# Optimization experiments

Measured on AMD Instinct MI355X. Metric: run time of the kernel, lower is better.

Reference implementation:

```python
import jax, jax.numpy as jnp
import numpy as np

B, S, D, E, K = 4, 2048, 1024, 8, 2
EPS, W_THRES, TEMP = 1e-4, 0.1, 1.0


def setup_inputs() -> dict:
    key = jax.random.key(0)
    k1, k2, k3, k4, k5 = jax.random.split(key, 5)
    x = jax.random.normal(k1, (B, S, D), dtype=jnp.float32)
    gate_W = jax.random.normal(k2, (D, E), dtype=jnp.float32) * 0.02
    gate_b = jnp.zeros((E,), dtype=jnp.float32)
    expert_W = jax.random.normal(k3, (E, D, D), dtype=jnp.float32) * 0.02
    expert_b = jnp.zeros((E, D), dtype=jnp.float32)
    return {"x": x, "gate_W": gate_W, "gate_b": gate_b,
            "expert_W": expert_W, "expert_b": expert_b}


def reference(x, gate_W, gate_b, expert_W, expert_b):
    # Gating: linear -> temperature -> clamp-min(eps) -> softmax
    scores = jnp.maximum((x @ gate_W + gate_b) / TEMP, EPS)      # [B,S,E]
    p = jax.nn.softmax(scores, axis=-1)                           # [B,S,E]
    _, topk_idx = jax.lax.top_k(p, K)                             # [B,S,K]
    # boolean membership mask of selected experts
    topk_mask = jax.nn.one_hot(topk_idx, E, dtype=p.dtype).sum(-2) > 0  # [B,S,E]
    # weights: clamp-min(weight_thres), normalized by detached sum over selected
    w = jnp.maximum(p, W_THRES)                                   # [B,S,E]
    w_gather = jnp.take_along_axis(w, topk_idx, axis=-1)          # [B,S,K]
    total = jax.lax.stop_gradient(w_gather.sum(-1, keepdims=True))
    w = w / total
    comb = jnp.where(topk_mask, w, jnp.zeros_like(w))             # [B,S,E]
    # Dense equivalent of gather/expert/scatter loop (E small): each expert
    # is Linear(D, D); masked combine weights zero out unselected experts.
    y = jnp.einsum('bsd,edf->bsef', x, expert_W) + expert_b       # [B,S,E,D]
    out = jnp.einsum('bsef,bse->bsf', y, comb) / K                # [B,S,D]
    return out
```

## Files before the change

kernel.cpp:

```cpp
#include <hip/hip_runtime.h>
#include <hip/hip_fp16.h>
#include <stdint.h>

#define TOK 8192
#define DIM 1024
#define NE 8
#define NT 72
#define NCT 8

typedef short bf16x8 __attribute__((ext_vector_type(8)));
typedef float f32x4 __attribute__((ext_vector_type(4)));

__device__ __forceinline__ unsigned short f2bf(float f) {
  unsigned int u = __float_as_uint(f);
  u += 0x7FFFu + ((u >> 16) & 1u);
  return (unsigned short)(u >> 16);
}

__device__ __forceinline__ void gl_lds16(const void* g, void* l) {
  __builtin_amdgcn_global_load_lds(
      (__attribute__((address_space(1))) unsigned int*)(g),
      (__attribute__((address_space(3))) unsigned int*)(l), 16, 0, 0);
}

__device__ __forceinline__ unsigned lds_off(const void* p) {
  return (unsigned)(size_t)(__attribute__((address_space(3))) const void*)p;
}

__global__ __launch_bounds__(256) void gate_kernel(
    const float* __restrict__ x, const float* __restrict__ gW,
    const float* __restrict__ gb, unsigned short* __restrict__ xb,
    int* __restrict__ eSel, float* __restrict__ wSel, int* __restrict__ cnt)
{
  if (blockIdx.x == 0 && threadIdx.x < NE) cnt[threadIdx.x] = 0;

  __shared__ float gWs[NE * DIM];
#pragma unroll
  for (int h = 0; h < 8; ++h) {
    const int m = threadIdx.x + h * 256;
    float4 v = ((const float4*)gW)[m];
    const int d = m >> 1, e0 = (m & 1) * 4;
    gWs[(e0 + 0) * DIM + d] = v.x;
    gWs[(e0 + 1) * DIM + d] = v.y;
    gWs[(e0 + 2) * DIM + d] = v.z;
    gWs[(e0 + 3) * DIM + d] = v.w;
  }
  __syncthreads();

  const int wave = threadIdx.x >> 6;
  const int lane = threadIdx.x & 63;
  const int t = blockIdx.x * 4 + wave;
  const float4* xrow = (const float4*)(x + (size_t)t * DIM);
  ushort4* xbrow = (ushort4*)(xb + (size_t)t * DIM);

  double acc[NE];
#pragma unroll
  for (int e = 0; e < NE; ++e) acc[e] = 0.0;

#pragma unroll
  for (int i = 0; i < 4; ++i) {
    const int j = i * 64 + lane;
    float4 v = xrow[j];
    ushort4 pk;
    pk.x = f2bf(v.x); pk.y = f2bf(v.y); pk.z = f2bf(v.z); pk.w = f2bf(v.w);
    xbrow[j] = pk;
#pragma unroll
    for (int e = 0; e < NE; ++e) {
      float4 gv = *(const float4*)&gWs[e * DIM + j * 4];
      acc[e] += (double)v.x * (double)gv.x + (double)v.y * (double)gv.y
              + (double)v.z * (double)gv.z + (double)v.w * (double)gv.w;
    }
  }
#pragma unroll
  for (int off = 32; off > 0; off >>= 1) {
#pragma unroll
    for (int e = 0; e < NE; ++e)
      acc[e] += __shfl_xor(acc[e], off, 64);
  }

  if (lane == 0) {
    double s[NE];
#pragma unroll
    for (int e = 0; e < NE; ++e) {
      s[e] = acc[e] + (double)gb[e];
      if (s[e] < 1e-4) s[e] = 1e-4;
    }
    int e0 = 0;
    for (int e = 1; e < NE; ++e) if (s[e] > s[e0]) e0 = e;
    int e1 = (e0 == 0) ? 1 : 0;
    for (int e = 0; e < NE; ++e) if (e != e0 && s[e] > s[e1]) e1 = e;
    float m = (float)s[e0];
    float Z = 0.f, pf[NE];
#pragma unroll
    for (int e = 0; e < NE; ++e) { pf[e] = __expf((float)s[e] - m); Z += pf[e]; }
    float w0 = pf[e0] / Z; if (w0 < 0.1f) w0 = 0.1f;
    float w1 = pf[e1] / Z; if (w1 < 0.1f) w1 = 0.1f;
    const float inv = 0.5f / (w0 + w1);
    eSel[t * 2 + 0] = e0;
    eSel[t * 2 + 1] = e1;
    wSel[t * 2 + 0] = w0 * inv;
    wSel[t * 2 + 1] = w1 * inv;
  }
}

__global__ __launch_bounds__(256) void scatter_kernel(
    const int* __restrict__ eSel, const float* __restrict__ wSel,
    int* __restrict__ cnt, int* __restrict__ listTok, float* __restrict__ listW)
{
  __shared__ int lcnt[NE];
  __shared__ int base[NE];
  const int tid = threadIdx.x;
  if (tid < NE) lcnt[tid] = 0;
  __syncthreads();

  const int t = blockIdx.x * 256 + tid;
  const int e0 = eSel[t * 2 + 0];
  const int e1 = eSel[t * 2 + 1];
  const float w0 = wSel[t * 2 + 0];
  const float w1 = wSel[t * 2 + 1];
  const int l0 = atomicAdd(&lcnt[e0], 1);
  const int l1 = atomicAdd(&lcnt[e1], 1);
  __syncthreads();
  if (tid < NE) base[tid] = atomicAdd(&cnt[tid], lcnt[tid]);
  __syncthreads();

  const int p0 = base[e0] + l0;
  listTok[e0 * TOK + p0] = t * 2 + 0;
  listW [e0 * TOK + p0] = w0;
  const int p1 = base[e1] + l1;
  listTok[e1 * TOK + p1] = t * 2 + 1;
  listW [e1 * TOK + p1] = w1;
}

__global__ __launch_bounds__(256) void transpose_w(
    const float* __restrict__ W, unsigned short* __restrict__ Wt)
{
  __shared__ float t2[64][65];
  const int b  = blockIdx.x;
  const int e  = b >> 8;
  const int db = (b >> 4) & 15;
  const int fb = b & 15;
  const int d0 = db * 64, f0 = fb * 64;
  const int tid = threadIdx.x;
#pragma unroll
  for (int h = 0; h < 4; ++h) {
    const int idx = tid + h * 256;
    const int r = idx >> 4, c4 = idx & 15;
    float4 v = *(const float4*)&W[((size_t)e * DIM + d0 + r) * DIM + f0 + c4 * 4];
    t2[r][c4 * 4 + 0] = v.x;
    t2[r][c4 * 4 + 1] = v.y;
    t2[r][c4 * 4 + 2] = v.z;
    t2[r][c4 * 4 + 3] = v.w;
  }
  __syncthreads();
#pragma unroll
  for (int h = 0; h < 8; ++h) {
    const int o = tid + h * 256;
    const int f = o >> 5, k2 = (o & 31) * 2;
    const unsigned int lo = f2bf(t2[k2][f]);
    const unsigned int hi = f2bf(t2[k2 + 1][f]);
    *(unsigned int*)&Wt[((size_t)e * DIM + f0 + f) * DIM + d0 + k2] =
        lo | (hi << 16);
  }
}

#define WAITVM(n) asm volatile("s_waitcnt vmcnt(" #n ")" ::: "memory")

#define STG(kt, bs)                                                          \
  { const int off_ = (kt) * 32;                                              \
    gl_lds16(srcA0 + off_, &As[bs][w * 2048 + 0]);                           \
    gl_lds16(srcA1 + off_, &As[bs][w * 2048 + 512]);                         \
    gl_lds16(srcA2 + off_, &As[bs][w * 2048 + 1024]);                        \
    gl_lds16(srcA3 + off_, &As[bs][w * 2048 + 1536]);                        \
    gl_lds16(srcB0 + off_, &Bs[bs][w * 1024 + 0]);                           \
    gl_lds16(srcB1 + off_, &Bs[bs][w * 1024 + 512]); }

#define CMP(bs)                                                              \
  { const unsigned aA = asOff + (unsigned)(bs) * 16384u + rdA2;              \
    const unsigned bA = bsOff + (unsigned)(bs) * 8192u + rdB2;               \
    bf16x8 a0,a1,a2,a3,a4,a5,a6,a7,b0,b1,b2,b3;                              \
    asm volatile(                                                            \
      "ds_read_b128 %0, %12 offset:0\n\t"                                    \
      "ds_read_b128 %1, %12 offset:1024\n\t"                                 \
      "ds_read_b128 %2, %12 offset:2048\n\t"                                 \
      "ds_read_b128 %3, %12 offset:3072\n\t"                                 \
      "ds_read_b128 %4, %12 offset:4096\n\t"                                 \
      "ds_read_b128 %5, %12 offset:5120\n\t"                                 \
      "ds_read_b128 %6, %12 offset:6144\n\t"                                 \
      "ds_read_b128 %7, %12 offset:7168\n\t"                                 \
      "ds_read_b128 %8, %13 offset:0\n\t"                                    \
      "ds_read_b128 %9, %13 offset:1024\n\t"                                 \
      "ds_read_b128 %10, %13 offset:2048\n\t"                                \
      "ds_read_b128 %11, %13 offset:3072\n\t"                                \
      "s_waitcnt lgkmcnt(0)"                                                 \
      : "=&v"(a0),"=&v"(a1),"=&v"(a2),"=&v"(a3),                             \
        "=&v"(a4),"=&v"(a5),"=&v"(a6),"=&v"(a7),                             \
        "=&v"(b0),"=&v"(b1),"=&v"(b2),"=&v"(b3)                              \
      : "v"(aA), "v"(bA)                                                     \
      : "memory");                                                           \
    __builtin_amdgcn_sched_barrier(0);                                       \
    bf16x8 af[8] = {a0, a1, a2, a3, a4, a5, a6, a7};                         \
    bf16x8 bfr[4] = {b0, b1, b2, b3};                                        \
    __builtin_amdgcn_s_setprio(1);                                           \
    _Pragma("unroll")                                                        \
    for (int mt = 0; mt < 8; ++mt)                                           \
      _Pragma("unroll")                                                      \
      for (int nt = 0; nt < 4; ++nt)                                         \
        acc[mt][nt] = __builtin_amdgcn_mfma_f32_16x16x32_bf16(               \
            af[mt], bfr[nt], acc[mt][nt], 0, 0, 0);                          \
    __builtin_amdgcn_s_setprio(0); }

__global__ __launch_bounds__(256, 2) void moe_gemm(
    const unsigned short* __restrict__ xb, const unsigned short* __restrict__ Wt,
    const float* __restrict__ eb, const int* __restrict__ cnt,
    const int* __restrict__ listTok, const float* __restrict__ listW,
    __half* __restrict__ yslot)
{
  const int dId = blockIdx.x % NT;
  const int cT  = blockIdx.x / NT;
  int e = -1, r0 = 0, rows = 0, accT = 0;
#pragma unroll
  for (int ee = 0; ee < NE; ++ee) {
    const int c = cnt[ee];
    const int nt = (c + 255) >> 8;
    if (dId >= accT && dId < accT + nt) {
      e = ee; r0 = (dId - accT) * 256;
      rows = c - r0; if (rows > 256) rows = 256;
    }
    accT += nt;
  }
  if (e < 0) return;

  __shared__ __align__(16) unsigned short As[3][256 * 32];
  __shared__ __align__(16) unsigned short Bs[3][128 * 32];
  __shared__ int   tid_s[256];
  __shared__ float w_s[256];

  const int tid = threadIdx.x;
  if (tid < rows) {
    tid_s[tid] = listTok[e * TOK + r0 + tid];
    w_s[tid]   = listW [e * TOK + r0 + tid];
  } else {
    tid_s[tid] = 0;
    w_s[tid]   = 0.0f;
  }
  __syncthreads();

  const int w    = tid >> 6;
  const int lane = tid & 63;
  const int qsrc = (lane & 3) ^ ((lane >> 3) & 3);
  const int lr   = lane >> 2;
  const unsigned short* srcA0 = xb + (size_t)(tid_s[w * 64 +  0 + lr] >> 1) * DIM + qsrc * 8;
  const unsigned short* srcA1 = xb + (size_t)(tid_s[w * 64 + 16 + lr] >> 1) * DIM + qsrc * 8;
  const unsigned short* srcA2 = xb + (size_t)(tid_s[w * 64 + 32 + lr] >> 1) * DIM + qsrc * 8;
  const unsigned short* srcA3 = xb + (size_t)(tid_s[w * 64 + 48 + lr] >> 1) * DIM + qsrc * 8;
  const unsigned short* srcB0 = Wt + ((size_t)e * DIM + cT * 128 + w * 32 +  0 + lr) * DIM + qsrc * 8;
  const unsigned short* srcB1 = Wt + ((size_t)e * DIM + cT * 128 + w * 32 + 16 + lr) * DIM + qsrc * 8;

  const int wr = w >> 1, wc = w & 1;
  const int mrow = lane & 15;
  const int qg   = lane >> 4;
  const int s8   = (qg ^ ((mrow >> 1) & 3)) * 8;
  const unsigned rdA2 = (unsigned)(((wr * 128 + mrow) * 32 + s8) * 2);
  const unsigned rdB2 = (unsigned)(((wc * 64 + mrow) * 32 + s8) * 2);
  const unsigned asOff = lds_off(&As[0][0]);
  const unsigned bsOff = lds_off(&Bs[0][0]);

  f32x4 acc[8][4];
#pragma unroll
  for (int i = 0; i < 8; ++i)
#pragma unroll
    for (int j = 0; j < 4; ++j)
      acc[i][j] = {0.f, 0.f, 0.f, 0.f};

  STG(0, 0);
  STG(1, 1);
  WAITVM(6);
  __builtin_amdgcn_s_barrier();

  int bC = 0, bS = 2;
#pragma unroll 1
  for (int kt = 0; kt < 30; ++kt) {
    STG(kt + 2, bS);
    CMP(bC);
    WAITVM(6);
    __builtin_amdgcn_s_barrier();
    bC = (bC == 2) ? 0 : bC + 1;
    bS = (bS == 2) ? 0 : bS + 1;
  }
  CMP(0);
  WAITVM(0);
  __builtin_amdgcn_s_barrier();
  CMP(1);

  const int colBase = cT * 128 + wc * 64 + mrow;
  float bias[4];
#pragma unroll
  for (int nt = 0; nt < 4; ++nt)
    bias[nt] = eb[(size_t)e * DIM + colBase + nt * 16];
#pragma unroll
  for (int mt = 0; mt < 8; ++mt) {
#pragma unroll
    for (int r = 0; r < 4; ++r) {
      const int rloc = wr * 128 + mt * 16 + (lane >> 4) * 4 + r;
      if (rloc < rows) {
        const int tk    = tid_s[rloc];
        const float wgt = w_s[rloc];
        __half* dst = yslot + ((size_t)(tk & 1) * TOK + (size_t)(tk >> 1)) * DIM;
#pragma unroll
        for (int nt = 0; nt < 4; ++nt)
          dst[colBase + nt * 16] = __float2half(wgt * (acc[mt][nt][r] + bias[nt]));
      }
    }
  }
}

__global__ __launch_bounds__(256) void combine(
    const __half* __restrict__ y0, const __half* __restrict__ y1,
    float4* __restrict__ out)
{
  const size_t i = (size_t)blockIdx.x * 256 + threadIdx.x;
  const ushort4 ua = ((const ushort4*)y0)[i];
  const ushort4 ub = ((const ushort4*)y1)[i];
  const __half* ah = (const __half*)&ua;
  const __half* bh = (const __half*)&ub;
  float4 o;
  o.x = __half2float(ah[0]) + __half2float(bh[0]);
  o.y = __half2float(ah[1]) + __half2float(bh[1]);
  o.z = __half2float(ah[2]) + __half2float(bh[2]);
  o.w = __half2float(ah[3]) + __half2float(bh[3]);
  out[i] = o;
}

extern "C" void kernel_launch(void* const* d_in, const int* in_sizes, int n_in,
                              void* d_out, int out_size, void* d_ws, size_t ws_size,
                              hipStream_t stream)
{
  const float* x  = (const float*)d_in[0];
  const float* gW = (const float*)d_in[1];
  const float* gb = (const float*)d_in[2];
  const float* eW = (const float*)d_in[3];
  const float* eb = (const float*)d_in[4];
  float* out = (float*)d_out;

  char* p = (char*)d_ws;
  unsigned short* xb = (unsigned short*)p;  p += (size_t)TOK * DIM * 2;
  unsigned short* Wt = (unsigned short*)p;  p += (size_t)NE * DIM * DIM * 2;
  __half* yslot = (__half*)p;               p += (size_t)2 * TOK * DIM * 2;
  int* cnt = (int*)p;                       p += 256;
  int* listTok = (int*)p;                   p += (size_t)NE * TOK * 4;
  float* listW = (float*)p;                 p += (size_t)NE * TOK * 4;

  int*   eSel = (int*)yslot;
  float* wSel = (float*)((char*)yslot + TOK * 8);

  gate_kernel<<<TOK / 4, 256, 0, stream>>>(x, gW, gb, xb, eSel, wSel, cnt);
  scatter_kernel<<<TOK / 256, 256, 0, stream>>>(eSel, wSel, cnt, listTok, listW);
  transpose_w<<<NE * 256, 256, 0, stream>>>(eW, Wt);
  moe_gemm<<<NT * NCT, 256, 0, stream>>>(xb, Wt, eb, cnt, listTok, listW, yslot);
  combine<<<TOK * DIM / 4 / 256, 256, 0, stream>>>(
      yslot, yslot + (size_t)TOK * DIM, (float4*)out);
}
```

Before: 198.8 us.

## Widen MoE GEMM tile to 256x256, double-buffer, and fuse transpose into gate

Each MoE GEMM block now computes 256 output columns instead of 128, halving column tiles and doubling per-wave accumulators to 8x8 MFMA tiles for more reuse of the A (token) data loaded from LDS. The LDS pipeline changes from triple buffering with two stages in flight to double buffering with a full vmcnt(0) wait each step. The LDS reads are split so half the MFMAs can start before all fragments arrive. The weight transpose kernel is merged into the gate kernel as extra blocks, saving one launch and letting both overlap. The larger accumulator raises register pressure at two blocks per CU, and the shallower prefetch may expose more memory latency.

```diff
diff --git a/kernel.cpp b/kernel.cpp
--- a/kernel.cpp
+++ b/kernel.cpp
@@ -6,7 +6,7 @@
 #define DIM 1024
 #define NE 8
 #define NT 72
-#define NCT 8
+#define NCT 4
 
 typedef short bf16x8 __attribute__((ext_vector_type(8)));
 typedef float f32x4 __attribute__((ext_vector_type(4)));
@@ -27,14 +27,48 @@
   return (unsigned)(size_t)(__attribute__((address_space(3))) const void*)p;
 }
 
-__global__ __launch_bounds__(256) void gate_kernel(
+__global__ __launch_bounds__(256) void gate_transpose(
     const float* __restrict__ x, const float* __restrict__ gW,
     const float* __restrict__ gb, unsigned short* __restrict__ xb,
-    int* __restrict__ eSel, float* __restrict__ wSel, int* __restrict__ cnt)
-{
+    int* __restrict__ eSel, float* __restrict__ wSel, int* __restrict__ cnt,
+    const float* __restrict__ W, unsigned short* __restrict__ Wt)
+{
+  __shared__ __align__(16) float smem[NE * DIM];
+
+  if (blockIdx.x >= 2048) {
+    float (*t2)[65] = (float(*)[65])smem;
+    const int b  = blockIdx.x - 2048;
+    const int e  = b >> 8;
+    const int db = (b >> 4) & 15;
+    const int fb = b & 15;
+    const int d0 = db * 64, f0 = fb * 64;
+    const int tid = threadIdx.x;
+#pragma unroll
+    for (int h = 0; h < 4; ++h) {
+      const int idx = tid + h * 256;
+      const int r = idx >> 4, c4 = idx & 15;
+      float4 v = *(const float4*)&W[((size_t)e * DIM + d0 + r) * DIM + f0 + c4 * 4];
+      t2[r][c4 * 4 + 0] = v.x;
+      t2[r][c4 * 4 + 1] = v.y;
+      t2[r][c4 * 4 + 2] = v.z;
+      t2[r][c4 * 4 + 3] = v.w;
+    }
+    __syncthreads();
+#pragma unroll
+    for (int h = 0; h < 8; ++h) {
+      const int o = tid + h * 256;
+      const int f = o >> 5, k2 = (o & 31) * 2;
+      const unsigned int lo = f2bf(t2[k2][f]);
+      const unsigned int hi = f2bf(t2[k2 + 1][f]);
+      *(unsigned int*)&Wt[((size_t)e * DIM + f0 + f) * DIM + d0 + k2] =
+          lo | (hi << 16);
+    }
+    return;
+  }
+
   if (blockIdx.x == 0 && threadIdx.x < NE) cnt[threadIdx.x] = 0;
 
-  __shared__ float gWs[NE * DIM];
+  float* gWs = smem;
 #pragma unroll
   for (int h = 0; h < 8; ++h) {
     const int m = threadIdx.x + h * 256;
@@ -132,38 +166,6 @@
   listW [e1 * TOK + p1] = w1;
 }
 
-__global__ __launch_bounds__(256) void transpose_w(
-    const float* __restrict__ W, unsigned short* __restrict__ Wt)
-{
-  __shared__ float t2[64][65];
-  const int b  = blockIdx.x;
-  const int e  = b >> 8;
-  const int db = (b >> 4) & 15;
-  const int fb = b & 15;
-  const int d0 = db * 64, f0 = fb * 64;
-  const int tid = threadIdx.x;
-#pragma unroll
-  for (int h = 0; h < 4; ++h) {
-    const int idx = tid + h * 256;
-    const int r = idx >> 4, c4 = idx & 15;
-    float4 v = *(const float4*)&W[((size_t)e * DIM + d0 + r) * DIM + f0 + c4 * 4];
-    t2[r][c4 * 4 + 0] = v.x;
-    t2[r][c4 * 4 + 1] = v.y;
-    t2[r][c4 * 4 + 2] = v.z;
-    t2[r][c4 * 4 + 3] = v.w;
-  }
-  __syncthreads();
-#pragma unroll
-  for (int h = 0; h < 8; ++h) {
-    const int o = tid + h * 256;
-    const int f = o >> 5, k2 = (o & 31) * 2;
-    const unsigned int lo = f2bf(t2[k2][f]);
-    const unsigned int hi = f2bf(t2[k2 + 1][f]);
-    *(unsigned int*)&Wt[((size_t)e * DIM + f0 + f) * DIM + d0 + k2] =
-        lo | (hi << 16);
-  }
-}
-
 #define WAITVM(n) asm volatile("s_waitcnt vmcnt(" #n ")" ::: "memory")
 
 #define STG(kt, bs)                                                          \
@@ -172,42 +174,60 @@
     gl_lds16(srcA1 + off_, &As[bs][w * 2048 + 512]);                         \
     gl_lds16(srcA2 + off_, &As[bs][w * 2048 + 1024]);                        \
     gl_lds16(srcA3 + off_, &As[bs][w * 2048 + 1536]);                        \
-    gl_lds16(srcB0 + off_, &Bs[bs][w * 1024 + 0]);                           \
-    gl_lds16(srcB1 + off_, &Bs[bs][w * 1024 + 512]); }
+    gl_lds16(srcB0 + off_, &Bs[bs][w * 2048 + 0]);                           \
+    gl_lds16(srcB1 + off_, &Bs[bs][w * 2048 + 512]);                         \
+    gl_lds16(srcB2 + off_, &Bs[bs][w * 2048 + 1024]);                        \
+    gl_lds16(srcB3 + off_, &Bs[bs][w * 2048 + 1536]); }
 
 #define CMP(bs)                                                              \
   { const unsigned aA = asOff + (unsigned)(bs) * 16384u + rdA2;              \
-    const unsigned bA = bsOff + (unsigned)(bs) * 8192u + rdB2;               \
-    bf16x8 a0,a1,a2,a3,a4,a5,a6,a7,b0,b1,b2,b3;                              \
+    const unsigned bA = bsOff + (unsigned)(bs) * 16384u + rdB2;              \
+    bf16x8 a0,a1,a2,a3,a4,a5,a6,a7,b0,b1,b2,b3,b4,b5,b6,b7;                  \
     asm volatile(                                                            \
-      "ds_read_b128 %0, %12 offset:0\n\t"                                    \
-      "ds_read_b128 %1, %12 offset:1024\n\t"                                 \
-      "ds_read_b128 %2, %12 offset:2048\n\t"                                 \
-      "ds_read_b128 %3, %12 offset:3072\n\t"                                 \
-      "ds_read_b128 %4, %12 offset:4096\n\t"                                 \
-      "ds_read_b128 %5, %12 offset:5120\n\t"                                 \
-      "ds_read_b128 %6, %12 offset:6144\n\t"                                 \
-      "ds_read_b128 %7, %12 offset:7168\n\t"                                 \
-      "ds_read_b128 %8, %13 offset:0\n\t"                                    \
-      "ds_read_b128 %9, %13 offset:1024\n\t"                                 \
-      "ds_read_b128 %10, %13 offset:2048\n\t"                                \
-      "ds_read_b128 %11, %13 offset:3072\n\t"                                \
-      "s_waitcnt lgkmcnt(0)"                                                 \
+      "ds_read_b128 %0, %16 offset:0\n\t"                                    \
+      "ds_read_b128 %1, %16 offset:1024\n\t"                                 \
+      "ds_read_b128 %2, %16 offset:2048\n\t"                                 \
+      "ds_read_b128 %3, %16 offset:3072\n\t"                                 \
+      "ds_read_b128 %8, %17 offset:0\n\t"                                    \
+      "ds_read_b128 %9, %17 offset:1024\n\t"                                 \
+      "ds_read_b128 %10, %17 offset:2048\n\t"                                \
+      "ds_read_b128 %11, %17 offset:3072\n\t"                                \
+      "ds_read_b128 %12, %17 offset:4096\n\t"                                \
+      "ds_read_b128 %13, %17 offset:5120\n\t"                                \
+      "ds_read_b128 %14, %17 offset:6144\n\t"                                \
+      "ds_read_b128 %15, %17 offset:7168\n\t"                                \
+      "ds_read_b128 %4, %16 offset:4096\n\t"                                 \
+      "ds_read_b128 %5, %16 offset:5120\n\t"                                 \
+      "ds_read_b128 %6, %16 offset:6144\n\t"                                 \
+      "ds_read_b128 %7, %16 offset:7168\n\t"                                 \
+      "s_waitcnt lgkmcnt(4)"                                                 \
       : "=&v"(a0),"=&v"(a1),"=&v"(a2),"=&v"(a3),                             \
         "=&v"(a4),"=&v"(a5),"=&v"(a6),"=&v"(a7),                             \
-        "=&v"(b0),"=&v"(b1),"=&v"(b2),"=&v"(b3)                              \
+        "=&v"(b0),"=&v"(b1),"=&v"(b2),"=&v"(b3),                             \
+        "=&v"(b4),"=&v"(b5),"=&v"(b6),"=&v"(b7)                              \
       : "v"(aA), "v"(bA)                                                     \
       : "memory");                                                           \
     __builtin_amdgcn_sched_barrier(0);                                       \
-    bf16x8 af[8] = {a0, a1, a2, a3, a4, a5, a6, a7};                         \
-    bf16x8 bfr[4] = {b0, b1, b2, b3};                                        \
+    bf16x8 afL[4] = {a0, a1, a2, a3};                                        \
+    bf16x8 afH[4] = {a4, a5, a6, a7};                                        \
+    bf16x8 bfr[8] = {b0, b1, b2, b3, b4, b5, b6, b7};                        \
     __builtin_amdgcn_s_setprio(1);                                           \
     _Pragma("unroll")                                                        \
-    for (int mt = 0; mt < 8; ++mt)                                           \
+    for (int mt = 0; mt < 4; ++mt)                                           \
       _Pragma("unroll")                                                      \
-      for (int nt = 0; nt < 4; ++nt)                                         \
+      for (int nt = 0; nt < 8; ++nt)                                         \
         acc[mt][nt] = __builtin_amdgcn_mfma_f32_16x16x32_bf16(               \
-            af[mt], bfr[nt], acc[mt][nt], 0, 0, 0);                          \
+            afL[mt], bfr[nt], acc[mt][nt], 0, 0, 0);                         \
+    __builtin_amdgcn_s_setprio(0);                                           \
+    asm volatile("s_waitcnt lgkmcnt(0)" ::: "memory");                       \
+    __builtin_amdgcn_sched_barrier(0);                                       \
+    __builtin_amdgcn_s_setprio(1);                                           \
+    _Pragma("unroll")                                                        \
+    for (int mt = 0; mt < 4; ++mt)                                           \
+      _Pragma("unroll")                                                      \
+      for (int nt = 0; nt < 8; ++nt)                                         \
+        acc[mt + 4][nt] = __builtin_amdgcn_mfma_f32_16x16x32_bf16(           \
+            afH[mt], bfr[nt], acc[mt + 4][nt], 0, 0, 0);                     \
     __builtin_amdgcn_s_setprio(0); }
 
 __global__ __launch_bounds__(256, 2) void moe_gemm(
@@ -231,8 +251,8 @@
   }
   if (e < 0) return;
 
-  __shared__ __align__(16) unsigned short As[3][256 * 32];
-  __shared__ __align__(16) unsigned short Bs[3][128 * 32];
+  __shared__ __align__(16) unsigned short As[2][256 * 32];
+  __shared__ __align__(16) unsigned short Bs[2][256 * 32];
   __shared__ int   tid_s[256];
   __shared__ float w_s[256];
 
@@ -254,49 +274,48 @@
   const unsigned short* srcA1 = xb + (size_t)(tid_s[w * 64 + 16 + lr] >> 1) * DIM + qsrc * 8;
   const unsigned short* srcA2 = xb + (size_t)(tid_s[w * 64 + 32 + lr] >> 1) * DIM + qsrc * 8;
   const unsigned short* srcA3 = xb + (size_t)(tid_s[w * 64 + 48 + lr] >> 1) * DIM + qsrc * 8;
-  const unsigned short* srcB0 = Wt + ((size_t)e * DIM + cT * 128 + w * 32 +  0 + lr) * DIM + qsrc * 8;
-  const unsigned short* srcB1 = Wt + ((size_t)e * DIM + cT * 128 + w * 32 + 16 + lr) * DIM + qsrc * 8;
+  const size_t bbase = ((size_t)e * DIM + cT * 256 + w * 64) * DIM;
+  const unsigned short* srcB0 = Wt + bbase + (size_t)( 0 + lr) * DIM + qsrc * 8;
+  const unsigned short* srcB1 = Wt + bbase + (size_t)(16 + lr) * DIM + qsrc * 8;
+  const unsigned short* srcB2 = Wt + bbase + (size_t)(32 + lr) * DIM + qsrc * 8;
+  const unsigned short* srcB3 = Wt + bbase + (size_t)(48 + lr) * DIM + qsrc * 8;
 
   const int wr = w >> 1, wc = w & 1;
   const int mrow = lane & 15;
   const int qg   = lane >> 4;
   const int s8   = (qg ^ ((mrow >> 1) & 3)) * 8;
   const unsigned rdA2 = (unsigned)(((wr * 128 + mrow) * 32 + s8) * 2);
-  const unsigned rdB2 = (unsigned)(((wc * 64 + mrow) * 32 + s8) * 2);
+  const unsigned rdB2 = (unsigned)(((wc * 128 + mrow) * 32 + s8) * 2);
   const unsigned asOff = lds_off(&As[0][0]);
   const unsigned bsOff = lds_off(&Bs[0][0]);
 
-  f32x4 acc[8][4];
+  f32x4 acc[8][8];
 #pragma unroll
   for (int i = 0; i < 8; ++i)
 #pragma unroll
-    for (int j = 0; j < 4; ++j)
+    for (int j = 0; j < 8; ++j)
       acc[i][j] = {0.f, 0.f, 0.f, 0.f};
 
   STG(0, 0);
-  STG(1, 1);
-  WAITVM(6);
-  __builtin_amdgcn_s_barrier();
-
-  int bC = 0, bS = 2;
-#pragma unroll 1
-  for (int kt = 0; kt < 30; ++kt) {
-    STG(kt + 2, bS);
-    CMP(bC);
-    WAITVM(6);
-    __builtin_amdgcn_s_barrier();
-    bC = (bC == 2) ? 0 : bC + 1;
-    bS = (bS == 2) ? 0 : bS + 1;
-  }
-  CMP(0);
   WAITVM(0);
   __builtin_amdgcn_s_barrier();
-  CMP(1);
-
-  const int colBase = cT * 128 + wc * 64 + mrow;
-  float bias[4];
-#pragma unroll
-  for (int nt = 0; nt < 4; ++nt)
+
+  int buf = 0;
+#pragma unroll 1
+  for (int kt = 0; kt < 32; ++kt) {
+    if (kt < 31) STG(kt + 1, buf ^ 1);
+    CMP(buf);
+    if (kt < 31) {
+      WAITVM(0);
+      __builtin_amdgcn_s_barrier();
+      buf ^= 1;
+    }
+  }
+
+  const int colBase = cT * 256 + wc * 128 + mrow;
+  float bias[8];
+#pragma unroll
+  for (int nt = 0; nt < 8; ++nt)
     bias[nt] = eb[(size_t)e * DIM + colBase + nt * 16];
 #pragma unroll
   for (int mt = 0; mt < 8; ++mt) {
@@ -308,7 +327,7 @@
         const float wgt = w_s[rloc];
         __half* dst = yslot + ((size_t)(tk & 1) * TOK + (size_t)(tk >> 1)) * DIM;
 #pragma unroll
-        for (int nt = 0; nt < 4; ++nt)
+        for (int nt = 0; nt < 8; ++nt)
           dst[colBase + nt * 16] = __float2half(wgt * (acc[mt][nt][r] + bias[nt]));
       }
     }
@@ -354,9 +373,8 @@
   int*   eSel = (int*)yslot;
   float* wSel = (float*)((char*)yslot + TOK * 8);
 
-  gate_kernel<<<TOK / 4, 256, 0, stream>>>(x, gW, gb, xb, eSel, wSel, cnt);
+  gate_transpose<<<4096, 256, 0, stream>>>(x, gW, gb, xb, eSel, wSel, cnt, eW, Wt);
   scatter_kernel<<<TOK / 256, 256, 0, stream>>>(eSel, wSel, cnt, listTok, listW);
-  transpose_w<<<NE * 256, 256, 0, stream>>>(eW, Wt);
   moe_gemm<<<NT * NCT, 256, 0, stream>>>(xb, Wt, eb, cnt, listTok, listW, yslot);
   combine<<<TOK * DIM / 4 / 256, 256, 0, stream>>>(
       yslot, yslot + (size_t)TOK * DIM, (float4*)out);
```

Result: slower. 483.3 us (+143.0%).

## Enlarge MoE GEMM tile to 256x256 with 8 waves and fuse weight transpose into gate

Applied to the files above, without the earlier changes.

The grouped GEMM now uses 512-thread blocks computing 256x256 output tiles (NCT halved to 4), so each staged A tile is reused across twice as many output columns and fewer blocks are launched. The LDS reads are split so the first half of the MFMAs can start after a partial lgkmcnt wait. The weight transpose kernel is merged into the gate kernel as extra blocks to remove one launch and let the two overlap. The larger tile doubles the B LDS buffers, and the 512-thread blocks with launch_bounds(512,2) may cut occupancy or raise register pressure.

```diff
diff --git a/kernel.cpp b/kernel.cpp
--- a/kernel.cpp
+++ b/kernel.cpp
@@ -6,7 +6,7 @@
 #define DIM 1024
 #define NE 8
 #define NT 72
-#define NCT 8
+#define NCT 4
 
 typedef short bf16x8 __attribute__((ext_vector_type(8)));
 typedef float f32x4 __attribute__((ext_vector_type(4)));
@@ -27,14 +27,48 @@
   return (unsigned)(size_t)(__attribute__((address_space(3))) const void*)p;
 }
 
-__global__ __launch_bounds__(256) void gate_kernel(
+__global__ __launch_bounds__(256) void gate_transpose(
     const float* __restrict__ x, const float* __restrict__ gW,
     const float* __restrict__ gb, unsigned short* __restrict__ xb,
-    int* __restrict__ eSel, float* __restrict__ wSel, int* __restrict__ cnt)
-{
+    int* __restrict__ eSel, float* __restrict__ wSel, int* __restrict__ cnt,
+    const float* __restrict__ W, unsigned short* __restrict__ Wt)
+{
+  __shared__ __align__(16) float smem[NE * DIM];
+
+  if (blockIdx.x >= 2048) {
+    float (*t2)[65] = (float(*)[65])smem;
+    const int b  = blockIdx.x - 2048;
+    const int e  = b >> 8;
+    const int db = (b >> 4) & 15;
+    const int fb = b & 15;
+    const int d0 = db * 64, f0 = fb * 64;
+    const int tid = threadIdx.x;
+#pragma unroll
+    for (int h = 0; h < 4; ++h) {
+      const int idx = tid + h * 256;
+      const int r = idx >> 4, c4 = idx & 15;
+      float4 v = *(const float4*)&W[((size_t)e * DIM + d0 + r) * DIM + f0 + c4 * 4];
+      t2[r][c4 * 4 + 0] = v.x;
+      t2[r][c4 * 4 + 1] = v.y;
+      t2[r][c4 * 4 + 2] = v.z;
+      t2[r][c4 * 4 + 3] = v.w;
+    }
+    __syncthreads();
+#pragma unroll
+    for (int h = 0; h < 8; ++h) {
+      const int o = tid + h * 256;
+      const int f = o >> 5, k2 = (o & 31) * 2;
+      const unsigned int lo = f2bf(t2[k2][f]);
+      const unsigned int hi = f2bf(t2[k2 + 1][f]);
+      *(unsigned int*)&Wt[((size_t)e * DIM + f0 + f) * DIM + d0 + k2] =
+          lo | (hi << 16);
+    }
+    return;
+  }
+
   if (blockIdx.x == 0 && threadIdx.x < NE) cnt[threadIdx.x] = 0;
 
-  __shared__ float gWs[NE * DIM];
+  float* gWs = smem;
 #pragma unroll
   for (int h = 0; h < 8; ++h) {
     const int m = threadIdx.x + h * 256;
@@ -132,85 +166,62 @@
   listW [e1 * TOK + p1] = w1;
 }
 
-__global__ __launch_bounds__(256) void transpose_w(
-    const float* __restrict__ W, unsigned short* __restrict__ Wt)
-{
-  __shared__ float t2[64][65];
-  const int b  = blockIdx.x;
-  const int e  = b >> 8;
-  const int db = (b >> 4) & 15;
-  const int fb = b & 15;
-  const int d0 = db * 64, f0 = fb * 64;
-  const int tid = threadIdx.x;
-#pragma unroll
-  for (int h = 0; h < 4; ++h) {
-    const int idx = tid + h * 256;
-    const int r = idx >> 4, c4 = idx & 15;
-    float4 v = *(const float4*)&W[((size_t)e * DIM + d0 + r) * DIM + f0 + c4 * 4];
-    t2[r][c4 * 4 + 0] = v.x;
-    t2[r][c4 * 4 + 1] = v.y;
-    t2[r][c4 * 4 + 2] = v.z;
-    t2[r][c4 * 4 + 3] = v.w;
-  }
-  __syncthreads();
-#pragma unroll
-  for (int h = 0; h < 8; ++h) {
-    const int o = tid + h * 256;
-    const int f = o >> 5, k2 = (o & 31) * 2;
-    const unsigned int lo = f2bf(t2[k2][f]);
-    const unsigned int hi = f2bf(t2[k2 + 1][f]);
-    *(unsigned int*)&Wt[((size_t)e * DIM + f0 + f) * DIM + d0 + k2] =
-        lo | (hi << 16);
-  }
-}
-
 #define WAITVM(n) asm volatile("s_waitcnt vmcnt(" #n ")" ::: "memory")
 
 #define STG(kt, bs)                                                          \
   { const int off_ = (kt) * 32;                                              \
-    gl_lds16(srcA0 + off_, &As[bs][w * 2048 + 0]);                           \
-    gl_lds16(srcA1 + off_, &As[bs][w * 2048 + 512]);                         \
-    gl_lds16(srcA2 + off_, &As[bs][w * 2048 + 1024]);                        \
-    gl_lds16(srcA3 + off_, &As[bs][w * 2048 + 1536]);                        \
-    gl_lds16(srcB0 + off_, &Bs[bs][w * 1024 + 0]);                           \
-    gl_lds16(srcB1 + off_, &Bs[bs][w * 1024 + 512]); }
+    gl_lds16(srcA0 + off_, &As[bs][w * 512]);                                \
+    gl_lds16(srcA1 + off_, &As[bs][128 * 32 + w * 512]);                     \
+    gl_lds16(srcB0 + off_, &Bs[bs][w * 512]);                                \
+    gl_lds16(srcB1 + off_, &Bs[bs][128 * 32 + w * 512]); }
 
 #define CMP(bs)                                                              \
   { const unsigned aA = asOff + (unsigned)(bs) * 16384u + rdA2;              \
-    const unsigned bA = bsOff + (unsigned)(bs) * 8192u + rdB2;               \
+    const unsigned bA = bsOff + (unsigned)(bs) * 16384u + rdB2;              \
     bf16x8 a0,a1,a2,a3,a4,a5,a6,a7,b0,b1,b2,b3;                              \
     asm volatile(                                                            \
       "ds_read_b128 %0, %12 offset:0\n\t"                                    \
       "ds_read_b128 %1, %12 offset:1024\n\t"                                 \
       "ds_read_b128 %2, %12 offset:2048\n\t"                                 \
       "ds_read_b128 %3, %12 offset:3072\n\t"                                 \
+      "ds_read_b128 %8, %13 offset:0\n\t"                                    \
+      "ds_read_b128 %9, %13 offset:1024\n\t"                                 \
+      "ds_read_b128 %10, %13 offset:2048\n\t"                                \
+      "ds_read_b128 %11, %13 offset:3072\n\t"                                \
       "ds_read_b128 %4, %12 offset:4096\n\t"                                 \
       "ds_read_b128 %5, %12 offset:5120\n\t"                                 \
       "ds_read_b128 %6, %12 offset:6144\n\t"                                 \
       "ds_read_b128 %7, %12 offset:7168\n\t"                                 \
-      "ds_read_b128 %8, %13 offset:0\n\t"                                    \
-      "ds_read_b128 %9, %13 offset:1024\n\t"                                 \
-      "ds_read_b128 %10, %13 offset:2048\n\t"                                \
-      "ds_read_b128 %11, %13 offset:3072\n\t"                                \
-      "s_waitcnt lgkmcnt(0)"                                                 \
+      "s_waitcnt lgkmcnt(4)"                                                 \
       : "=&v"(a0),"=&v"(a1),"=&v"(a2),"=&v"(a3),                             \
         "=&v"(a4),"=&v"(a5),"=&v"(a6),"=&v"(a7),                             \
         "=&v"(b0),"=&v"(b1),"=&v"(b2),"=&v"(b3)                              \
       : "v"(aA), "v"(bA)                                                     \
       : "memory");                                                           \
     __builtin_amdgcn_sched_barrier(0);                                       \
-    bf16x8 af[8] = {a0, a1, a2, a3, a4, a5, a6, a7};                         \
+    bf16x8 afL[4] = {a0, a1, a2, a3};                                        \
+    bf16x8 afH[4] = {a4, a5, a6, a7};                                        \
     bf16x8 bfr[4] = {b0, b1, b2, b3};                                        \
     __builtin_amdgcn_s_setprio(1);                                           \
     _Pragma("unroll")                                                        \
-    for (int mt = 0; mt < 8; ++mt)                                           \
+    for (int mt = 0; mt < 4; ++mt)                                           \
       _Pragma("unroll")                                                      \
       for (int nt = 0; nt < 4; ++nt)                                         \
         acc[mt][nt] = __builtin_amdgcn_mfma_f32_16x16x32_bf16(               \
-            af[mt], bfr[nt], acc[mt][nt], 0, 0, 0);                          \
+            afL[mt], bfr[nt], acc[mt][nt], 0, 0, 0);                         \
+    __builtin_amdgcn_s_setprio(0);                                           \
+    asm volatile("s_waitcnt lgkmcnt(0)" ::: "memory");                       \
+    __builtin_amdgcn_sched_barrier(0);                                       \
+    __builtin_amdgcn_s_setprio(1);                                           \
+    _Pragma("unroll")                                                        \
+    for (int mt = 0; mt < 4; ++mt)                                           \
+      _Pragma("unroll")                                                      \
+      for (int nt = 0; nt < 4; ++nt)                                         \
+        acc[mt + 4][nt] = __builtin_amdgcn_mfma_f32_16x16x32_bf16(           \
+            afH[mt], bfr[nt], acc[mt + 4][nt], 0, 0, 0);                     \
     __builtin_amdgcn_s_setprio(0); }
 
-__global__ __launch_bounds__(256, 2) void moe_gemm(
+__global__ __launch_bounds__(512, 2) void moe_gemm(
     const unsigned short* __restrict__ xb, const unsigned short* __restrict__ Wt,
     const float* __restrict__ eb, const int* __restrict__ cnt,
     const int* __restrict__ listTok, const float* __restrict__ listW,
@@ -232,17 +243,19 @@
   if (e < 0) return;
 
   __shared__ __align__(16) unsigned short As[3][256 * 32];
-  __shared__ __align__(16) unsigned short Bs[3][128 * 32];
+  __shared__ __align__(16) unsigned short Bs[3][256 * 32];
   __shared__ int   tid_s[256];
   __shared__ float w_s[256];
 
   const int tid = threadIdx.x;
-  if (tid < rows) {
-    tid_s[tid] = listTok[e * TOK + r0 + tid];
-    w_s[tid]   = listW [e * TOK + r0 + tid];
-  } else {
-    tid_s[tid] = 0;
-    w_s[tid]   = 0.0f;
+  if (tid < 256) {
+    if (tid < rows) {
+      tid_s[tid] = listTok[e * TOK + r0 + tid];
+      w_s[tid]   = listW [e * TOK + r0 + tid];
+    } else {
+      tid_s[tid] = 0;
+      w_s[tid]   = 0.0f;
+    }
   }
   __syncthreads();
 
@@ -250,14 +263,13 @@
   const int lane = tid & 63;
   const int qsrc = (lane & 3) ^ ((lane >> 3) & 3);
   const int lr   = lane >> 2;
-  const unsigned short* srcA0 = xb + (size_t)(tid_s[w * 64 +  0 + lr] >> 1) * DIM + qsrc * 8;
-  const unsigned short* srcA1 = xb + (size_t)(tid_s[w * 64 + 16 + lr] >> 1) * DIM + qsrc * 8;
-  const unsigned short* srcA2 = xb + (size_t)(tid_s[w * 64 + 32 + lr] >> 1) * DIM + qsrc * 8;
-  const unsigned short* srcA3 = xb + (size_t)(tid_s[w * 64 + 48 + lr] >> 1) * DIM + qsrc * 8;
-  const unsigned short* srcB0 = Wt + ((size_t)e * DIM + cT * 128 + w * 32 +  0 + lr) * DIM + qsrc * 8;
-  const unsigned short* srcB1 = Wt + ((size_t)e * DIM + cT * 128 + w * 32 + 16 + lr) * DIM + qsrc * 8;
-
-  const int wr = w >> 1, wc = w & 1;
+  const unsigned short* srcA0 = xb + (size_t)(tid_s[      w * 16 + lr] >> 1) * DIM + qsrc * 8;
+  const unsigned short* srcA1 = xb + (size_t)(tid_s[128 + w * 16 + lr] >> 1) * DIM + qsrc * 8;
+  const size_t bbase = ((size_t)e * DIM + cT * 256) * DIM;
+  const unsigned short* srcB0 = Wt + bbase + (size_t)(      w * 16 + lr) * DIM + qsrc * 8;
+  const unsigned short* srcB1 = Wt + bbase + (size_t)(128 + w * 16 + lr) * DIM + qsrc * 8;
+
+  const int wr = w >> 2, wc = w & 3;
   const int mrow = lane & 15;
   const int qg   = lane >> 4;
   const int s8   = (qg ^ ((mrow >> 1) & 3)) * 8;
@@ -275,25 +287,26 @@
 
   STG(0, 0);
   STG(1, 1);
-  WAITVM(6);
+  WAITVM(4);
   __builtin_amdgcn_s_barrier();
 
-  int bC = 0, bS = 2;
+  int sC = 0, sS = 2;
 #pragma unroll 1
-  for (int kt = 0; kt < 30; ++kt) {
-    STG(kt + 2, bS);
-    CMP(bC);
-    WAITVM(6);
-    __builtin_amdgcn_s_barrier();
-    bC = (bC == 2) ? 0 : bC + 1;
-    bS = (bS == 2) ? 0 : bS + 1;
-  }
-  CMP(0);
-  WAITVM(0);
-  __builtin_amdgcn_s_barrier();
-  CMP(1);
-
-  const int colBase = cT * 128 + wc * 64 + mrow;
+  for (int kt = 0; kt < 32; ++kt) {
+    if (kt < 30) STG(kt + 2, sS);
+    CMP(sC);
+    if (kt < 30) {
+      WAITVM(4);
+      __builtin_amdgcn_s_barrier();
+    } else if (kt == 30) {
+      WAITVM(0);
+      __builtin_amdgcn_s_barrier();
+    }
+    sC = (sC == 2) ? 0 : sC + 1;
+    sS = (sS == 2) ? 0 : sS + 1;
+  }
+
+  const int colBase = cT * 256 + wc * 64 + mrow;
   float bias[4];
 #pragma unroll
   for (int nt = 0; nt < 4; ++nt)
@@ -354,10 +367,9 @@
   int*   eSel = (int*)yslot;
   float* wSel = (float*)((char*)yslot + TOK * 8);
 
-  gate_kernel<<<TOK / 4, 256, 0, stream>>>(x, gW, gb, xb, eSel, wSel, cnt);
+  gate_transpose<<<4096, 256, 0, stream>>>(x, gW, gb, xb, eSel, wSel, cnt, eW, Wt);
   scatter_kernel<<<TOK / 256, 256, 0, stream>>>(eSel, wSel, cnt, listTok, listW);
-  transpose_w<<<NE * 256, 256, 0, stream>>>(eW, Wt);
-  moe_gemm<<<NT * NCT, 256, 0, stream>>>(xb, Wt, eb, cnt, listTok, listW, yslot);
+  moe_gemm<<<NT * NCT, 512, 0, stream>>>(xb, Wt, eb, cnt, listTok, listW, yslot);
   combine<<<TOK * DIM / 4 / 256, 256, 0, stream>>>(
       yslot, yslot + (size_t)TOK * DIM, (float4*)out);
 }
```

Measured after the change: 199.8 us. About the same (+0.5%).

## Fuse gate/transpose/zeroing launch, atomically accumulate expert outputs, split LDS wait

Applied to the files above, without the earlier changes.

Merges the gating, weight-transpose and output-zeroing work into one launch that dispatches on block index. The GEMM epilogue now does float atomic adds straight into the output, which removes the fp16 slot buffers and the separate combine kernel. The LDS read order is changed so the first half of the MFMAs can start after a partial lgkmcnt wait. This saves launches and the intermediate round-trip through memory. In exchange, scattered per-element atomics add traffic, the summation order becomes nondeterministic, and the fused kernel holds a larger shared allocation in every block.

```diff
diff --git a/kernel.cpp b/kernel.cpp
--- a/kernel.cpp
+++ b/kernel.cpp
@@ -27,14 +27,58 @@
   return (unsigned)(size_t)(__attribute__((address_space(3))) const void*)p;
 }
 
-__global__ __launch_bounds__(256) void gate_kernel(
+__global__ __launch_bounds__(256) void gate_transpose(
     const float* __restrict__ x, const float* __restrict__ gW,
     const float* __restrict__ gb, unsigned short* __restrict__ xb,
-    int* __restrict__ eSel, float* __restrict__ wSel, int* __restrict__ cnt)
+    int* __restrict__ eSel, float* __restrict__ wSel, int* __restrict__ cnt,
+    const float* __restrict__ W, unsigned short* __restrict__ Wt,
+    float4* __restrict__ outz)
 {
+  __shared__ __align__(16) float smem[NE * DIM];
+
+  if (blockIdx.x >= 4096) {
+    const float4 z = {0.f, 0.f, 0.f, 0.f};
+    const unsigned base = (blockIdx.x - 4096) * 256 + threadIdx.x;
+#pragma unroll
+    for (int h = 0; h < 4; ++h)
+      outz[base + h * 524288] = z;
+    return;
+  }
+
+  if (blockIdx.x >= 2048) {
+    float (*t2)[65] = (float(*)[65])smem;
+    const int b  = blockIdx.x - 2048;
+    const int e  = b >> 8;
+    const int db = (b >> 4) & 15;
+    const int fb = b & 15;
+    const int d0 = db * 64, f0 = fb * 64;
+    const int tid = threadIdx.x;
+#pragma unroll
+    for (int h = 0; h < 4; ++h) {
+      const int idx = tid + h * 256;
+      const int r = idx >> 4, c4 = idx & 15;
+      float4 v = *(const float4*)&W[((size_t)e * DIM + d0 + r) * DIM + f0 + c4 * 4];
+      t2[r][c4 * 4 + 0] = v.x;
+      t2[r][c4 * 4 + 1] = v.y;
+      t2[r][c4 * 4 + 2] = v.z;
+      t2[r][c4 * 4 + 3] = v.w;
+    }
+    __syncthreads();
+#pragma unroll
+    for (int h = 0; h < 8; ++h) {
+      const int o = tid + h * 256;
+      const int f = o >> 5, k2 = (o & 31) * 2;
+      const unsigned int lo = f2bf(t2[k2][f]);
+      const unsigned int hi = f2bf(t2[k2 + 1][f]);
+      *(unsigned int*)&Wt[((size_t)e * DIM + f0 + f) * DIM + d0 + k2] =
+          lo | (hi << 16);
+    }
+    return;
+  }
+
   if (blockIdx.x == 0 && threadIdx.x < NE) cnt[threadIdx.x] = 0;
 
-  __shared__ float gWs[NE * DIM];
+  float* gWs = smem;
 #pragma unroll
   for (int h = 0; h < 8; ++h) {
     const int m = threadIdx.x + h * 256;
@@ -130,38 +174,6 @@
   const int p1 = base[e1] + l1;
   listTok[e1 * TOK + p1] = t * 2 + 1;
   listW [e1 * TOK + p1] = w1;
-}
-
-__global__ __launch_bounds__(256) void transpose_w(
-    const float* __restrict__ W, unsigned short* __restrict__ Wt)
-{
-  __shared__ float t2[64][65];
-  const int b  = blockIdx.x;
-  const int e  = b >> 8;
-  const int db = (b >> 4) & 15;
-  const int fb = b & 15;
-  const int d0 = db * 64, f0 = fb * 64;
-  const int tid = threadIdx.x;
-#pragma unroll
-  for (int h = 0; h < 4; ++h) {
-    const int idx = tid + h * 256;
-    const int r = idx >> 4, c4 = idx & 15;
-    float4 v = *(const float4*)&W[((size_t)e * DIM + d0 + r) * DIM + f0 + c4 * 4];
-    t2[r][c4 * 4 + 0] = v.x;
-    t2[r][c4 * 4 + 1] = v.y;
-    t2[r][c4 * 4 + 2] = v.z;
-    t2[r][c4 * 4 + 3] = v.w;
-  }
-  __syncthreads();
-#pragma unroll
-  for (int h = 0; h < 8; ++h) {
-    const int o = tid + h * 256;
-    const int f = o >> 5, k2 = (o & 31) * 2;
-    const unsigned int lo = f2bf(t2[k2][f]);
-    const unsigned int hi = f2bf(t2[k2 + 1][f]);
-    *(unsigned int*)&Wt[((size_t)e * DIM + f0 + f) * DIM + d0 + k2] =
-        lo | (hi << 16);
-  }
 }
 
 #define WAITVM(n) asm volatile("s_waitcnt vmcnt(" #n ")" ::: "memory")
@@ -184,37 +196,48 @@
       "ds_read_b128 %1, %12 offset:1024\n\t"                                 \
       "ds_read_b128 %2, %12 offset:2048\n\t"                                 \
       "ds_read_b128 %3, %12 offset:3072\n\t"                                 \
+      "ds_read_b128 %8, %13 offset:0\n\t"                                    \
+      "ds_read_b128 %9, %13 offset:1024\n\t"                                 \
+      "ds_read_b128 %10, %13 offset:2048\n\t"                                \
+      "ds_read_b128 %11, %13 offset:3072\n\t"                                \
       "ds_read_b128 %4, %12 offset:4096\n\t"                                 \
       "ds_read_b128 %5, %12 offset:5120\n\t"                                 \
       "ds_read_b128 %6, %12 offset:6144\n\t"                                 \
       "ds_read_b128 %7, %12 offset:7168\n\t"                                 \
-      "ds_read_b128 %8, %13 offset:0\n\t"                                    \
-      "ds_read_b128 %9, %13 offset:1024\n\t"                                 \
-      "ds_read_b128 %10, %13 offset:2048\n\t"                                \
-      "ds_read_b128 %11, %13 offset:3072\n\t"                                \
-      "s_waitcnt lgkmcnt(0)"                                                 \
+      "s_waitcnt lgkmcnt(4)"                                                 \
       : "=&v"(a0),"=&v"(a1),"=&v"(a2),"=&v"(a3),                             \
         "=&v"(a4),"=&v"(a5),"=&v"(a6),"=&v"(a7),                             \
         "=&v"(b0),"=&v"(b1),"=&v"(b2),"=&v"(b3)                              \
       : "v"(aA), "v"(bA)                                                     \
       : "memory");                                                           \
     __builtin_amdgcn_sched_barrier(0);                                       \
-    bf16x8 af[8] = {a0, a1, a2, a3, a4, a5, a6, a7};                         \
+    bf16x8 afL[4] = {a0, a1, a2, a3};                                        \
     bf16x8 bfr[4] = {b0, b1, b2, b3};                                        \
     __builtin_amdgcn_s_setprio(1);                                           \
     _Pragma("unroll")                                                        \
-    for (int mt = 0; mt < 8; ++mt)                                           \
+    for (int mt = 0; mt < 4; ++mt)                                           \
       _Pragma("unroll")                                                      \
       for (int nt = 0; nt < 4; ++nt)                                         \
         acc[mt][nt] = __builtin_amdgcn_mfma_f32_16x16x32_bf16(               \
-            af[mt], bfr[nt], acc[mt][nt], 0, 0, 0);                          \
+            afL[mt], bfr[nt], acc[mt][nt], 0, 0, 0);                         \
+    __builtin_amdgcn_s_setprio(0);                                           \
+    asm volatile("s_waitcnt lgkmcnt(0)" ::: "memory");                       \
+    __builtin_amdgcn_sched_barrier(0);                                       \
+    bf16x8 afH[4] = {a4, a5, a6, a7};                                        \
+    __builtin_amdgcn_s_setprio(1);                                           \
+    _Pragma("unroll")                                                        \
+    for (int mt = 0; mt < 4; ++mt)                                           \
+      _Pragma("unroll")                                                      \
+      for (int nt = 0; nt < 4; ++nt)                                         \
+        acc[mt + 4][nt] = __builtin_amdgcn_mfma_f32_16x16x32_bf16(           \
+            afH[mt], bfr[nt], acc[mt + 4][nt], 0, 0, 0);                     \
     __builtin_amdgcn_s_setprio(0); }
 
 __global__ __launch_bounds__(256, 2) void moe_gemm(
     const unsigned short* __restrict__ xb, const unsigned short* __restrict__ Wt,
     const float* __restrict__ eb, const int* __restrict__ cnt,
     const int* __restrict__ listTok, const float* __restrict__ listW,
-    __half* __restrict__ yslot)
+    float* __restrict__ out)
 {
   const int dId = blockIdx.x % NT;
   const int cT  = blockIdx.x / NT;
@@ -306,30 +329,14 @@
       if (rloc < rows) {
         const int tk    = tid_s[rloc];
         const float wgt = w_s[rloc];
-        __half* dst = yslot + ((size_t)(tk & 1) * TOK + (size_t)(tk >> 1)) * DIM;
+        float* dst = out + (size_t)(tk >> 1) * DIM;
 #pragma unroll
         for (int nt = 0; nt < 4; ++nt)
-          dst[colBase + nt * 16] = __float2half(wgt * (acc[mt][nt][r] + bias[nt]));
+          unsafeAtomicAdd(&dst[colBase + nt * 16],
+                          wgt * (acc[mt][nt][r] + bias[nt]));
       }
     }
   }
-}
-
-__global__ __launch_bounds__(256) void combine(
-    const __half* __restrict__ y0, const __half* __restrict__ y1,
-    float4* __restrict__ out)
-{
-  const size_t i = (size_t)blockIdx.x * 256 + threadIdx.x;
-  const ushort4 ua = ((const ushort4*)y0)[i];
-  const ushort4 ub = ((const ushort4*)y1)[i];
-  const __half* ah = (const __half*)&ua;
-  const __half* bh = (const __half*)&ub;
-  float4 o;
-  o.x = __half2float(ah[0]) + __half2float(bh[0]);
-  o.y = __half2float(ah[1]) + __half2float(bh[1]);
-  o.z = __half2float(ah[2]) + __half2float(bh[2]);
-  o.w = __half2float(ah[3]) + __half2float(bh[3]);
-  out[i] = o;
 }
 
 extern "C" void kernel_launch(void* const* d_in, const int* in_sizes, int n_in,
@@ -346,18 +353,16 @@
   char* p = (char*)d_ws;
   unsigned short* xb = (unsigned short*)p;  p += (size_t)TOK * DIM * 2;
   unsigned short* Wt = (unsigned short*)p;  p += (size_t)NE * DIM * DIM * 2;
-  __half* yslot = (__half*)p;               p += (size_t)2 * TOK * DIM * 2;
+  char* scratch = p;                        p += (size_t)2 * TOK * DIM * 2;
   int* cnt = (int*)p;                       p += 256;
   int* listTok = (int*)p;                   p += (size_t)NE * TOK * 4;
   float* listW = (float*)p;                 p += (size_t)NE * TOK * 4;
 
-  int*   eSel = (int*)yslot;
-  float* wSel = (float*)((char*)yslot + TOK * 8);
-
-  gate_kernel<<<TOK / 4, 256, 0, stream>>>(x, gW, gb, xb, eSel, wSel, cnt);
+  int*   eSel = (int*)scratch;
+  float* wSel = (float*)(scratch + TOK * 8);
+
+  gate_transpose<<<6144, 256, 0, stream>>>(x, gW, gb, xb, eSel, wSel, cnt,
+                                           eW, Wt, (float4*)out);
   scatter_kernel<<<TOK / 256, 256, 0, stream>>>(eSel, wSel, cnt, listTok, listW);
-  transpose_w<<<NE * 256, 256, 0, stream>>>(eW, Wt);
-  moe_gemm<<<NT * NCT, 256, 0, stream>>>(xb, Wt, eb, cnt, listTok, listW, yslot);
-  combine<<<TOK * DIM / 4 / 256, 256, 0, stream>>>(
-      yslot, yslot + (size_t)TOK * DIM, (float4*)out);
-}
+  moe_gemm<<<NT * NCT, 256, 0, stream>>>(xb, Wt, eb, cnt, listTok, listW, out);
+}
```

Result: slower. 222.1 us (+11.7%).
